# Kernel optimization log

Hardware: AMD Instinct MI355X
Metric: run time of the kernel (lower is better)

The kernel has to match this reference:

```python
import jax, jax.numpy as jnp
import numpy as np

N_NODES, N_EDGES, NNZ = 10000, 4000, 30000
IN_CH, HEADS, OUT_CH = 128, 2, 64


def _scale2_pattern(node, edge, num_nodes, num_edges):
    """Sparsity pattern of H @ (H^T H) where H is the node x edge incidence.
    Mirrors torch.sparse.mm + coalesce + (values > 0) mask (pattern only,
    since all values are positive sums of ones)."""
    # unique incidence pattern (coalesce)
    uk = np.unique(node.astype(np.int64) * num_edges + edge.astype(np.int64))
    n_u, e_u = uk // num_edges, uk % num_edges
    # --- stage 1: pattern of H^T H = edge pairs sharing a node ---
    order = np.argsort(n_u, kind="stable")
    ns, es = n_u[order], e_u[order]
    _, starts, cnts = np.unique(ns, return_index=True, return_counts=True)
    cpe = np.repeat(cnts, cnts)          # group size per sorted entry
    gpe = np.repeat(starts, cnts)        # group start per sorted entry
    tot = int(cpe.sum())
    within = np.arange(tot) - np.repeat(np.cumsum(cpe) - cpe, cpe)
    pe = np.repeat(es, cpe)
    pep = es[np.repeat(gpe, cpe) + within]
    pk = np.unique(pe * num_edges + pep)
    pe, pep = pk // num_edges, pk % num_edges
    # --- stage 2: pattern of H @ (H^T H) ---
    po = np.argsort(pe, kind="stable")
    pe_s, pep_s = pe[po], pep[po]
    cnt_e = np.bincount(pe_s, minlength=num_edges)
    ptr = np.concatenate([np.zeros(1, np.int64), np.cumsum(cnt_e)])
    c2 = cnt_e[e_u]
    tot2 = int(c2.sum())
    within2 = np.arange(tot2) - np.repeat(np.cumsum(c2) - c2, c2)
    v2 = np.repeat(n_u, c2)
    ep2 = pep_s[ptr[e_u].repeat(c2) + within2]
    k2 = np.unique(v2 * num_edges + ep2)
    return k2 // num_edges, k2 % num_edges


def setup_inputs() -> dict:
    rng = np.random.default_rng(0)
    node1 = rng.integers(0, N_NODES, NNZ).astype(np.int64)
    edge1 = rng.integers(0, N_EDGES, NNZ).astype(np.int64)
    node2, edge2 = _scale2_pattern(node1, edge1, N_NODES, N_EDGES)

    key = jax.random.key(0)
    k = jax.random.split(key, 4)
    HO = HEADS * OUT_CH
    xav1 = (2.0 / (IN_CH + HO)) ** 0.5
    xavo = (2.0 / (HO + OUT_CH)) ** 0.5
    return {
        "x": jax.random.normal(k[0], (N_NODES, IN_CH), jnp.float32),
        "hyperedge_index1": jnp.asarray(np.stack([node1, edge1]), jnp.int32),
        "hyperedge_index2": jnp.asarray(np.stack([node2, edge2]), jnp.int32),
        "W1": jax.random.normal(k[1], (HO, IN_CH), jnp.float32) * xav1,
        "b1": jnp.zeros((HO,), jnp.float32),
        "W2": jax.random.normal(k[2], (HO, IN_CH), jnp.float32) * xav1,
        "b2": jnp.zeros((HO,), jnp.float32),
        "Wout": jax.random.normal(k[3], (OUT_CH, HO), jnp.float32) * xavo,
        "bout": jnp.zeros((OUT_CH,), jnp.float32),
        "num_edges": N_EDGES,
    }


def _hconv(x, W, b, node_idx, edge_idx, num_edges):
    num_nodes = x.shape[0]
    xt = x @ W.T + b                                  # [N, H*O]
    g = xt[node_idx]                                  # [nnz, H*O] gather
    esum = jax.ops.segment_sum(g, edge_idx, num_segments=num_edges)
    cnt = jax.ops.segment_sum(jnp.ones(edge_idx.shape, xt.dtype), edge_idx,
                              num_segments=num_edges)
    emean = esum / jnp.maximum(cnt, 1.0)[:, None]     # scatter_mean (0 if empty)
    return jax.ops.segment_sum(emean[edge_idx], node_idx,
                               num_segments=num_nodes)  # scatter_add


def reference(x, hyperedge_index1, hyperedge_index2, W1, b1, W2, b2, Wout, bout,
              num_edges):
    o1 = _hconv(x, W1, b1, hyperedge_index1[0], hyperedge_index1[1], num_edges)
    o2 = _hconv(x, W2, b2, hyperedge_index2[0], hyperedge_index2[1], num_edges)
    o = 0.5 * (o1 + o2)                               # mean over 2 scales
    return o @ Wout.T + bout                          # output_proj
```

## Files before the change

### kernel.cpp

```cpp
#include <hip/hip_runtime.h>
#include <hip/hip_bf16.h>

#define N_NODES 10000
#define N_EDGES 4000
#define IN_CH   128
#define CHUNK   16384

#define G_GEMM  625
#define G_NPTR  40

__device__ __forceinline__ float bf2f(unsigned short u) {
    union { unsigned int i; float f; } v;
    v.i = ((unsigned int)u) << 16;
    return v.f;
}
__device__ __forceinline__ unsigned short f2bfu(float f) {
    union { __hip_bfloat16 h; unsigned short u; } v;
    v.h = __float2bfloat16(f);
    return v.u;
}

__device__ __forceinline__ void load8(const void* base, size_t eoff, int isf32,
                                      float o[8]) {
    if (isf32) {
        const float4* q = (const float4*)((const float*)base + eoff);
        float4 a = q[0], b = q[1];
        o[0]=a.x; o[1]=a.y; o[2]=a.z; o[3]=a.w;
        o[4]=b.x; o[5]=b.y; o[6]=b.z; o[7]=b.w;
    } else {
        uint4 v = *(const uint4*)((const unsigned short*)base + eoff);
        const unsigned short* pv = (const unsigned short*)&v;
#pragma unroll
        for (int q = 0; q < 8; q++) o[q] = bf2f(pv[q]);
    }
}

__device__ __forceinline__ float loadS(const void* base, int i, int isf32) {
    return isf32 ? ((const float*)base)[i] : bf2f(((const unsigned short*)base)[i]);
}

__device__ __forceinline__ int probe_isf32(const unsigned int* __restrict__ x) {
    const int lane = threadIdx.x & 63;
    unsigned int w0 = x[lane * 2], w1 = x[lane * 2 + 1];
    int h = 0, z = 0;
    {
        unsigned int lo = w0 & 0xFFFFu;
        if (lo == 0u) z++; else if (((lo >> 7) & 0xFF) >= 0x90u) h++;
        lo = w1 & 0xFFFFu;
        if (lo == 0u) z++; else if (((lo >> 7) & 0xFF) >= 0x90u) h++;
    }
    unsigned long long bh = __ballot(h > 0);
    unsigned long long bz = __ballot(z == 2);
    return (__popcll(bh) > 8 || __popcll(bz) > 50) ? 1 : 0;
}

__device__ __forceinline__ void add4(float acc[4], uint2 u) {
    acc[0] += bf2f((unsigned short)(u.x & 0xFFFFu));
    acc[1] += bf2f((unsigned short)(u.x >> 16));
    acc[2] += bf2f((unsigned short)(u.y & 0xFFFFu));
    acc[3] += bf2f((unsigned short)(u.y >> 16));
}

__device__ __forceinline__ void block_scan1024(const int* __restrict__ cnt,
                                               int nb, int* __restrict__ out,
                                               int* __restrict__ part)
{
    const int t = threadIdx.x;
    const int K = (nb + 1023) >> 10;
    const int base = t * K;
    int s = 0;
    for (int q = 0; q < K; q++) { int i = base + q; s += (i < nb) ? cnt[i] : 0; }
    part[t] = s;
    __syncthreads();
    for (int d = 1; d < 1024; d <<= 1) {
        int v = (t >= d) ? part[t - d] : 0;
        __syncthreads();
        part[t] += v;
        __syncthreads();
    }
    int run = part[t] - s;
    for (int q = 0; q < K; q++) {
        int i = base + q;
        if (i < nb) { out[i] = run; run += cnt[i]; }
    }
    if (t == 1023) out[nb] = part[1023];
    __syncthreads();
}

__global__ __launch_bounds__(256) void weff_zero(
    const void* __restrict__ Wout,
    const void* __restrict__ W1, const void* __restrict__ b1,
    const void* __restrict__ W2, const void* __restrict__ b2,
    float* __restrict__ weff1, float* __restrict__ beff1,
    float* __restrict__ weff2, float* __restrict__ beff2,
    int* __restrict__ cntz, int* __restrict__ fillz,
    const unsigned int* __restrict__ xprobe)
{
    const int b = blockIdx.x;
    if (b == 4) {
        for (int t = threadIdx.x; t < 18000; t += 256) cntz[t] = 0;
        for (int t = threadIdx.x; t < 14000; t += 256) fillz[t] = 0;
        return;
    }
    __shared__ float wsh[64][IN_CH];
    const int isf32 = probe_isf32(xprobe);

    if (b == 5) {
        float* bsh = &wsh[0][0];
        const int t = threadIdx.x;
        {
            const int s = t >> 7, h = t & 127;
            bsh[t] = loadS(s ? b2 : b1, h, isf32);
        }
        __syncthreads();
        if (t < 128) {
            const int s = t >> 6, o = t & 63;
            float a = 0.f;
#pragma unroll 4
            for (int r = 0; r < 16; r++) {
                float v[8];
                load8(Wout, (size_t)o * 128 + r * 8, isf32, v);
#pragma unroll
                for (int q = 0; q < 8; q++) a += v[q] * bsh[s * 128 + r * 8 + q];
            }
            (s ? beff2 : beff1)[o] = 0.5f * a;
        }
        return;
    }

    const int s  = b >> 1;
    const int oh = b & 1;
    const void* Ws = s ? W2 : W1;
    float* outW = s ? weff2 : weff1;
    const int o  = oh * 32 + (threadIdx.x >> 3);
    const int i0 = (threadIdx.x & 7) * 16;
    float acc[16];
#pragma unroll
    for (int k = 0; k < 16; k++) acc[k] = 0.f;

    for (int pass = 0; pass < 2; pass++) {
        if (pass) __syncthreads();
        for (int r = 0; r < 4; r++) {
            int idx = r * 2048 + threadIdx.x * 8;
            float v[8];
            load8(Ws, (size_t)pass * 8192 + idx, isf32, v);
            float* d = &wsh[0][0] + idx;
#pragma unroll
            for (int q = 0; q < 8; q++) d[q] = v[q];
        }
        float wrow[64];
#pragma unroll
        for (int r = 0; r < 8; r++) {
            float v[8];
            load8(Wout, (size_t)o * 128 + pass * 64 + r * 8, isf32, v);
#pragma unroll
            for (int q = 0; q < 8; q++) wrow[r * 8 + q] = v[q];
        }
        __syncthreads();
#pragma unroll 4
        for (int h = 0; h < 64; h++) {
            const float wo = wrow[h];
            const float* wr = &wsh[h][i0];
#pragma unroll
            for (int k = 0; k < 16; k++) acc[k] += wo * wr[k];
        }
    }
#pragma unroll
    for (int k = 0; k < 16; k++)
        outW[o * 128 + i0 + k] = 0.5f * acc[k];
}

__global__ __launch_bounds__(256) void prep(
    const void* __restrict__ x,
    const float* __restrict__ weff1, const float* __restrict__ beff1,
    const float* __restrict__ weff2, const float* __restrict__ beff2,
    unsigned short* __restrict__ xtP1b, unsigned short* __restrict__ xtP2b,
    const int* __restrict__ idx1, int nnz1,
    const int* __restrict__ idx2, int nnz2,
    int* __restrict__ nptr,
    int* __restrict__ bh, int* __restrict__ cnt2,
    int* __restrict__ cnt1e, int* __restrict__ cnt1n, int nblk)
{
    __shared__ __align__(16) char smem[40000];
    int b = blockIdx.x;

    if (b < nblk) {
        int* h = (int*)smem;
        for (int t = threadIdx.x; t < N_EDGES; t += 256) h[t] = 0;
        __syncthreads();
        const int lo = b * CHUNK;
        const int hi = min(nnz2, lo + CHUNK);
        for (int i = lo + threadIdx.x; i < hi; i += 256)
            atomicAdd(&h[idx2[nnz2 + i]], 1);
        __syncthreads();
        int* dst = bh + (size_t)b * N_EDGES;
        for (int t = threadIdx.x; t < N_EDGES; t += 256) {
            int v = h[t];
            dst[t] = v;
            if (v) atomicAdd(&cnt2[t], v);
        }
        return;
    }
    b -= nblk;

    if (b < 8) {
        const int isEdge = b < 4;
        const int bid = isEdge ? b : (b - 4);
        const int nb = isEdge ? N_EDGES : N_NODES;
        const int* src = isEdge ? (idx1 + nnz1) : idx1;
        int* dst = isEdge ? cnt1e : cnt1n;
        int* h = (int*)smem;
        for (int t = threadIdx.x; t < nb; t += 256) h[t] = 0;
        __syncthreads();
        for (int i = bid * 256 + threadIdx.x; i < nnz1; i += 4 * 256)
            atomicAdd(&h[src[i]], 1);
        __syncthreads();
        for (int t = threadIdx.x; t < nb; t += 256) {
            int v = h[t];
            if (v) atomicAdd(&dst[t], v);
        }
        return;
    }
    b -= 8;

    if (b < G_GEMM) {
        const int isf32 = probe_isf32((const unsigned int*)x);
        float (*xs)[IN_CH] = (float (*)[IN_CH])smem;
        const int n0 = b * 16;
        {
            float v[8];
            load8(x, (size_t)n0 * IN_CH + (size_t)threadIdx.x * 8, isf32, v);
            float* dst = &xs[0][0] + threadIdx.x * 8;
#pragma unroll
            for (int q = 0; q < 8; q++) dst[q] = v[q];
        }
        __syncthreads();

        const int g   = threadIdx.x >> 7;
        const int sel = (threadIdx.x >> 6) & 1;
        const int j   = threadIdx.x & 63;
        const float* WE = sel ? weff2 : weff1;
        const float* BE = sel ? beff2 : beff1;
        unsigned short* xtP = sel ? xtP2b : xtP1b;

        float acc[8];
#pragma unroll
        for (int m = 0; m < 8; m++) acc[m] = 0.f;

        const float4* Wr = (const float4*)(WE + (size_t)j * 128);
        for (int kk = 0; kk < 16; kk++) {
            float4 a = Wr[kk * 2], c = Wr[kk * 2 + 1];
            float w[8] = {a.x, a.y, a.z, a.w, c.x, c.y, c.z, c.w};
#pragma unroll
            for (int m = 0; m < 8; m++) {
                const float* xr = &xs[g * 8 + m][kk * 8];
                acc[m] += xr[0]*w[0] + xr[1]*w[1] + xr[2]*w[2] + xr[3]*w[3]
                        + xr[4]*w[4] + xr[5]*w[5] + xr[6]*w[6] + xr[7]*w[7];
            }
        }
        const float bias = BE[j];
#pragma unroll
        for (int m = 0; m < 8; m++)
            xtP[(size_t)(n0 + g * 8 + m) * 64 + j] = f2bfu(acc[m] + bias);
        return;
    }
    b -= G_GEMM;

    {
        int n = b * 256 + threadIdx.x;
        if (n > N_NODES) return;
        int lo = 0, hi = nnz2;
        while (lo < hi) { int mid = (lo + hi) >> 1; if (idx2[mid] < n) lo = mid + 1; else hi = mid; }
        nptr[n] = lo;
    }
}

__global__ __launch_bounds__(1024) void sort_fill(
    const int* __restrict__ cnt2, int* __restrict__ ptr2g,
    const int* __restrict__ bh, int nblk,
    const int* __restrict__ idx2, int nnz2,
    unsigned short* __restrict__ nodelist2,
    const int* __restrict__ idx1, int nnz1,
    const int* __restrict__ cnt1e, int* __restrict__ ptr1eg,
    int* __restrict__ fill1e, unsigned short* __restrict__ nodelist1,
    const int* __restrict__ cnt1n, int* __restrict__ ptr1ng,
    int* __restrict__ fill1n, unsigned short* __restrict__ edgelist1)
{
    __shared__ int sscan[14002];
    __shared__ int part[1024];
    int b = blockIdx.x;
    const int t = threadIdx.x;

    if (b < nblk) {
        block_scan1024(cnt2, N_EDGES, sscan, part);
        if (b == 0)
            for (int i = t; i <= N_EDGES; i += 1024) ptr2g[i] = sscan[i];
        int* lh = sscan + 4001;
        for (int e = t; e < N_EDGES; e += 1024) {
            int acc = sscan[e];
            for (int k = 0; k < b; k++) acc += bh[(size_t)k * N_EDGES + e];
            sscan[e] = acc;
            lh[e] = 0;
        }
        __syncthreads();
        const int lo = b * CHUNK;
        const int hi = min(nnz2, lo + CHUNK);
        for (int i = lo + t; i < hi; i += 1024) {
            int n = idx2[i];
            int e = idx2[nnz2 + i];
            int s = atomicAdd(&lh[e], 1);
            nodelist2[sscan[e] + s] = (unsigned short)n;
        }
        return;
    }
    b -= nblk;
    int* p1e = sscan;
    int* p1n = sscan + 4001;
    block_scan1024(cnt1e, N_EDGES, p1e, part);
    block_scan1024(cnt1n, N_NODES, p1n, part);
    if (b == 0) {
        for (int i = t; i <= N_EDGES; i += 1024) ptr1eg[i] = p1e[i];
        for (int i = t; i <= N_NODES; i += 1024) ptr1ng[i] = p1n[i];
    }
    int i = b * 1024 + t;
    if (i >= nnz1) return;
    int n = idx1[i];
    int e = idx1[nnz1 + i];
    int se = atomicAdd(&fill1e[e], 1);
    nodelist1[p1e[e] + se] = (unsigned short)n;
    int sn = atomicAdd(&fill1n[n], 1);
    edgelist1[p1n[n] + sn] = (unsigned short)e;
}

__global__ __launch_bounds__(256) void edge_gather(
    const unsigned short* __restrict__ nodelist2, const int* __restrict__ ptr2,
    const unsigned int* __restrict__ xtP2u, unsigned int* __restrict__ emean2b,
    const unsigned short* __restrict__ nodelist1, const int* __restrict__ ptr1e,
    const unsigned int* __restrict__ xtP1u, unsigned int* __restrict__ emean1b)
{
    int b = blockIdx.x;
    if (b < 1000) {
        const int lane = threadIdx.x & 63;
        const int sub  = lane >> 4;
        const int ch4  = lane & 15;
        const int e = b * 4 + (threadIdx.x >> 6);
        const int lo = ptr2[e], hi = ptr2[e + 1];
        const uint2* src2 = (const uint2*)xtP2u;
        float acc[4] = {0.f, 0.f, 0.f, 0.f};
        int i = lo;
        for (; i + 32 <= hi; i += 32) {
            int n[8]; uint2 u[8];
#pragma unroll
            for (int q = 0; q < 8; q++) n[q] = nodelist2[i + 4 * q + sub];
#pragma unroll
            for (int q = 0; q < 8; q++) u[q] = src2[(size_t)n[q] * 16 + ch4];
#pragma unroll
            for (int q = 0; q < 8; q++) add4(acc, u[q]);
        }
        for (; i < hi; i += 4) {
            if (i + sub < hi) {
                int n0 = nodelist2[i + sub];
                add4(acc, src2[(size_t)n0 * 16 + ch4]);
            }
        }
#pragma unroll
        for (int q = 0; q < 4; q++) {
            acc[q] += __shfl_xor(acc[q], 16);
            acc[q] += __shfl_xor(acc[q], 32);
        }
        if (sub == 0) {
            const float inv = 1.f / fmaxf((float)(hi - lo), 1.f);
            uint2 o;
            o.x = ((unsigned int)f2bfu(acc[1] * inv) << 16) | f2bfu(acc[0] * inv);
            o.y = ((unsigned int)f2bfu(acc[3] * inv) << 16) | f2bfu(acc[2] * inv);
            ((uint2*)emean2b)[(size_t)e * 16 + ch4] = o;
        }
        return;
    }
    b -= 1000;
    {
        const int lane = threadIdx.x & 31;
        const int e = b * 8 + (threadIdx.x >> 5);
        const int lo = ptr1e[e], hi = ptr1e[e + 1];
        float accx = 0.f, accy = 0.f;
        for (int base = lo; base < hi; base += 32) {
            const int m = min(32, hi - base);
            int vl = (base + lane < hi) ? (int)nodelist1[base + lane] : 0;
            int t = 0;
            for (; t + 7 < m; t += 8) {
                int nn[8]; unsigned int uu[8];
#pragma unroll
                for (int q = 0; q < 8; q++) nn[q] = __shfl(vl, t + q, 32);
#pragma unroll
                for (int q = 0; q < 8; q++) uu[q] = xtP1u[nn[q] * 32 + lane];
#pragma unroll
                for (int q = 0; q < 8; q++) {
                    accx += bf2f((unsigned short)(uu[q] & 0xFFFFu));
                    accy += bf2f((unsigned short)(uu[q] >> 16));
                }
            }
            for (; t < m; t++) {
                int n = __shfl(vl, t, 32);
                unsigned int u = xtP1u[n * 32 + lane];
                accx += bf2f((unsigned short)(u & 0xFFFFu));
                accy += bf2f((unsigned short)(u >> 16));
            }
        }
        const float inv = 1.f / fmaxf((float)(hi - lo), 1.f);
        emean1b[e * 32 + lane] =
            ((unsigned int)f2bfu(accy * inv) << 16) | f2bfu(accx * inv);
    }
}

__global__ __launch_bounds__(256) void node_final(
    const int* __restrict__ vals2, const int* __restrict__ nptr,
    const unsigned int* __restrict__ emean2b,
    const unsigned short* __restrict__ edgelist1, const int* __restrict__ ptr1n,
    const unsigned int* __restrict__ emean1b,
    const void* __restrict__ bout, void* __restrict__ out,
    const unsigned int* __restrict__ xprobe)
{
    const int isf32 = probe_isf32(xprobe);
    const int lane = threadIdx.x & 63;
    const int sub  = lane >> 4;
    const int ch4  = lane & 15;
    const int n = blockIdx.x * 4 + (threadIdx.x >> 6);
    float acc[4] = {0.f, 0.f, 0.f, 0.f};

    {
        const int lo = nptr[n], hi = nptr[n + 1];
        const uint2* src = (const uint2*)emean2b;
        int i = lo;
        for (; i + 32 <= hi; i += 32) {
            int e[8]; uint2 u[8];
#pragma unroll
            for (int q = 0; q < 8; q++) e[q] = vals2[i + 4 * q + sub];
#pragma unroll
            for (int q = 0; q < 8; q++) u[q] = src[(size_t)e[q] * 16 + ch4];
#pragma unroll
            for (int q = 0; q < 8; q++) add4(acc, u[q]);
        }
        for (; i < hi; i += 4) {
            if (i + sub < hi)
                add4(acc, src[(size_t)vals2[i + sub] * 16 + ch4]);
        }
    }
    {
        const int lo = ptr1n[n], hi = ptr1n[n + 1];
        const uint2* src = (const uint2*)emean1b;
        int i = lo;
        for (; i + 32 <= hi; i += 32) {
            int e[8]; uint2 u[8];
#pragma unroll
            for (int q = 0; q < 8; q++) e[q] = edgelist1[i + 4 * q + sub];
#pragma unroll
            for (int q = 0; q < 8; q++) u[q] = src[(size_t)e[q] * 16 + ch4];
#pragma unroll
            for (int q = 0; q < 8; q++) add4(acc, u[q]);
        }
        for (; i < hi; i += 4) {
            if (i + sub < hi)
                add4(acc, src[(size_t)edgelist1[i + sub] * 16 + ch4]);
        }
    }
#pragma unroll
    for (int q = 0; q < 4; q++) {
        acc[q] += __shfl_xor(acc[q], 16);
        acc[q] += __shfl_xor(acc[q], 32);
    }
    if (sub == 0) {
        float r[4];
#pragma unroll
        for (int q = 0; q < 4; q++)
            r[q] = acc[q] + loadS(bout, ch4 * 4 + q, isf32);
        if (isf32) {
            ((float4*)out)[(size_t)n * 16 + ch4] =
                make_float4(r[0], r[1], r[2], r[3]);
        } else {
            uint2 o;
            o.x = ((unsigned int)f2bfu(r[1]) << 16) | f2bfu(r[0]);
            o.y = ((unsigned int)f2bfu(r[3]) << 16) | f2bfu(r[2]);
            ((uint2*)out)[(size_t)n * 16 + ch4] = o;
        }
    }
}

extern "C" void kernel_launch(void* const* d_in, const int* in_sizes, int n_in,
                              void* d_out, int out_size, void* d_ws, size_t ws_size,
                              hipStream_t stream)
{
    const void* x  = d_in[0];
    const int* idx1 = (const int*)d_in[1];
    const int* idx2 = (const int*)d_in[2];
    const void* W1 = d_in[3];
    const void* b1 = d_in[4];
    const void* W2 = d_in[5];
    const void* b2 = d_in[6];
    const void* Wo = d_in[7];
    const void* bo = d_in[8];

    const int nnz1 = in_sizes[1] / 2;
    const int nnz2 = in_sizes[2] / 2;
    const int nblk = (nnz2 + CHUNK - 1) / CHUNK;
    const int F1p = (nnz1 + 1023) / 1024;

    float* ws = (float*)d_ws;
    unsigned short* xtP1b = (unsigned short*)ws;
    unsigned int*   xtP1u = (unsigned int*)xtP1b;
    unsigned short* xtP2b = (unsigned short*)(ws + 320000);
    unsigned int*   xtP2u = (unsigned int*)xtP2b;
    int*   fill1e = (int*)(ws + 1280000);
    int*   fill1n = (int*)(ws + 1284000);
    int* cnt2  = (int*)(ws + 1550000);
    int* cnt1e = (int*)(ws + 1554000);
    int* cnt1n = (int*)(ws + 1558000);
    int* ptr2  = (int*)(ws + 1568000);
    int* ptr1e = (int*)(ws + 1572004);
    int* ptr1n = (int*)(ws + 1576008);
    int* nptr  = (int*)(ws + 1586012);
    float* weff1 = ws + 1596016;
    float* weff2 = ws + 1604208;
    float* beff1 = ws + 1612400;
    float* beff2 = ws + 1612464;
    unsigned int* emean2b = (unsigned int*)(ws + 1612528);
    unsigned int* emean1b = (unsigned int*)(ws + 1740528);
    unsigned short* nodelist2 = (unsigned short*)(ws + 1868528);
    const size_t nl2u = ((size_t)nnz2 + 1) / 2;
    unsigned short* nodelist1 = (unsigned short*)(ws + 1868528 + nl2u);
    const size_t nl1u = ((size_t)nnz1 + 1) / 2;
    unsigned short* edgelist1 = (unsigned short*)(ws + 1868528 + nl2u + nl1u);
    const size_t bh_off = (1868528 + nl2u + 2 * nl1u + 7) & ~(size_t)7;
    int* bh = (int*)(ws + bh_off);

    weff_zero<<<6, 256, 0, stream>>>(Wo, W1, b1, W2, b2,
                                     weff1, beff1, weff2, beff2,
                                     cnt2, fill1e, (const unsigned int*)x);

    prep<<<nblk + 8 + G_GEMM + G_NPTR, 256, 0, stream>>>(
        x, weff1, beff1, weff2, beff2, xtP1b, xtP2b,
        idx1, nnz1, idx2, nnz2,
        nptr, bh, cnt2, cnt1e, cnt1n, nblk);

    sort_fill<<<nblk + F1p, 1024, 0, stream>>>(
        cnt2, ptr2, bh, nblk,
        idx2, nnz2, nodelist2,
        idx1, nnz1,
        cnt1e, ptr1e, fill1e, nodelist1,
        cnt1n, ptr1n, fill1n, edgelist1);

    edge_gather<<<1000 + N_EDGES / 8, 256, 0, stream>>>(
        nodelist2, ptr2, xtP2u, emean2b,
        nodelist1, ptr1e, xtP1u, emean1b);

    node_final<<<N_NODES / 4, 256, 0, stream>>>(
        idx2 + nnz2, nptr, emean2b, edgelist1, ptr1n, emean1b,
        bo, d_out, (const unsigned int*)x);
}
```

Measured before the change: 187.5 us.

## Use wave-shuffle block scan and smaller sort chunks

Replaces the shared-memory Hillis-Steele block scan, which needed about 20 barriers, with a two-level scan using wavefront shuffles plus a 16-entry shared scan of per-wave sums. Separately, it shrinks CHUNK so the fill stage is split across more blocks, raising parallelism in sort_fill. More chunks also mean more per-block histogram prefix work (the loop over bh rows grows with block index) and more histogram storage. The histogram kernel elsewhere must agree with the new CHUNK.

```diff
diff --git a/kernel.cpp b/kernel.cpp
--- a/kernel.cpp
+++ b/kernel.cpp
@@ -4,7 +4,7 @@
 #define N_NODES 10000
 #define N_EDGES 4000
 #define IN_CH   128
-#define CHUNK   16384
+#define CHUNK   4096
 
 #define G_GEMM  625
 #define G_NPTR  40
@@ -63,27 +63,39 @@
 
 __device__ __forceinline__ void block_scan1024(const int* __restrict__ cnt,
                                                int nb, int* __restrict__ out,
-                                               int* __restrict__ part)
+                                               int* __restrict__ wsum)
 {
     const int t = threadIdx.x;
+    const int lane = t & 63, wid = t >> 6;
     const int K = (nb + 1023) >> 10;
     const int base = t * K;
     int s = 0;
     for (int q = 0; q < K; q++) { int i = base + q; s += (i < nb) ? cnt[i] : 0; }
-    part[t] = s;
+    int inc = s;
+#pragma unroll
+    for (int d = 1; d < 64; d <<= 1) {
+        int v = __shfl_up(inc, d);
+        if (lane >= d) inc += v;
+    }
+    if (lane == 63) wsum[wid] = inc;
     __syncthreads();
-    for (int d = 1; d < 1024; d <<= 1) {
-        int v = (t >= d) ? part[t - d] : 0;
-        __syncthreads();
-        part[t] += v;
-        __syncthreads();
-    }
-    int run = part[t] - s;
+    if (t < 16) {
+        int v = wsum[t];
+#pragma unroll
+        for (int d = 1; d < 16; d <<= 1) {
+            int u = __shfl_up(v, d);
+            if (t >= d) v += u;
+        }
+        wsum[t] = v;
+    }
+    __syncthreads();
+    const int wbase = (wid == 0) ? 0 : wsum[wid - 1];
+    int run = wbase + inc - s;
     for (int q = 0; q < K; q++) {
         int i = base + q;
         if (i < nb) { out[i] = run; run += cnt[i]; }
     }
-    if (t == 1023) out[nb] = part[1023];
+    if (t == 1023) out[nb] = wsum[15];
     __syncthreads();
 }
 
@@ -287,12 +299,12 @@
     int* __restrict__ fill1n, unsigned short* __restrict__ edgelist1)
 {
     __shared__ int sscan[14002];
-    __shared__ int part[1024];
+    __shared__ int wsum[16];
     int b = blockIdx.x;
     const int t = threadIdx.x;
 
     if (b < nblk) {
-        block_scan1024(cnt2, N_EDGES, sscan, part);
+        block_scan1024(cnt2, N_EDGES, sscan, wsum);
         if (b == 0)
             for (int i = t; i <= N_EDGES; i += 1024) ptr2g[i] = sscan[i];
         int* lh = sscan + 4001;
@@ -316,8 +328,8 @@
     b -= nblk;
     int* p1e = sscan;
     int* p1n = sscan + 4001;
-    block_scan1024(cnt1e, N_EDGES, p1e, part);
-    block_scan1024(cnt1n, N_NODES, p1n, part);
+    block_scan1024(cnt1e, N_EDGES, p1e, wsum);
+    block_scan1024(cnt1n, N_NODES, p1n, wsum);
     if (b == 0) {
         for (int i = t; i <= N_EDGES; i += 1024) ptr1eg[i] = p1e[i];
         for (int i = t; i <= N_NODES; i += 1024) ptr1ng[i] = p1n[i];
```

New measurement: 207.8 us. 1.11x slower.
